# Kernel tuning notes

Hardware: AMD Instinct MI355X
Metric: run time of the kernel (lower is better)

Reference implementation:

```python
import jax, jax.numpy as jnp
import numpy as np

DIM = 128
POS_HID = 64
ATT_HID = DIM * 2
B, N = 4, 512


def _linear_init(key, fan_in, fan_out):
    # mimic torch Linear default init scale: U(-1/sqrt(fan_in), 1/sqrt(fan_in))
    kw, kb = jax.random.split(key)
    bound = 1.0 / np.sqrt(fan_in)
    W = jax.random.uniform(kw, (fan_in, fan_out), minval=-bound, maxval=bound, dtype=jnp.float32)
    b = jax.random.uniform(kb, (fan_out,), minval=-bound, maxval=bound, dtype=jnp.float32)
    return W, b


def setup_inputs() -> dict:
    key = jax.random.key(0)
    ks = jax.random.split(key, 6)
    x = jax.random.normal(ks[0], (B, DIM, N), dtype=jnp.float32)
    pos = jax.random.normal(ks[1], (B, N, 3), dtype=jnp.float32)
    Wqkv, bqkv = _linear_init(ks[2], DIM, DIM * 3)
    pW1, pb1 = _linear_init(ks[3], 3, POS_HID)
    pW2, pb2 = _linear_init(ks[4], POS_HID, DIM)
    k5a, k5b = jax.random.split(ks[5])
    aW1, ab1 = _linear_init(k5a, DIM, ATT_HID)
    aW2, ab2 = _linear_init(k5b, ATT_HID, DIM)
    return {"x": x, "pos": pos, "Wqkv": Wqkv, "bqkv": bqkv,
            "pW1": pW1, "pb1": pb1, "pW2": pW2, "pb2": pb2,
            "aW1": aW1, "ab1": ab1, "aW2": aW2, "ab2": ab2}


def reference(x, pos, Wqkv, bqkv, pW1, pb1, pW2, pb2, aW1, ab1, aW2, ab2):
    # x: [b, d, n] -> [b, n, d]
    xt = jnp.transpose(x, (0, 2, 1))
    qkv = xt @ Wqkv + bqkv                      # [b, n, 3d]
    q, k, v = jnp.split(qkv, 3, axis=-1)        # each [b, n, d]

    # pairwise relative positions: [b, i, j, 3]
    rel_pos = pos[:, :, None, :] - pos[:, None, :, :]
    # pos_mlp: Linear(3, hid) -> ReLU -> Linear(hid, d)
    rel_pos_emb = jax.nn.relu(rel_pos @ pW1 + pb1) @ pW2 + pb2   # [b, i, j, d]

    qk_rel = q[:, :, None, :] - k[:, None, :, :]                 # [b, i, j, d]
    v_ij = v[:, None, :, :] + rel_pos_emb                        # [b, i, j, d]

    # attn_mlp: Linear(d, 2d) -> ReLU -> Linear(2d, d)
    sim = jax.nn.relu((qk_rel + rel_pos_emb) @ aW1 + ab1) @ aW2 + ab2  # [b, i, j, d]
    attn = jax.nn.softmax(sim, axis=2)                           # softmax over j (dim=-2)
    agg = jnp.sum(attn * v_ij, axis=2)                           # [b, i, d]
    return jnp.transpose(agg, (0, 2, 1))                         # [b, d, n]
```

## Files before the change

### kernel.cpp

```cpp
#include <hip/hip_runtime.h>
#include <hip/hip_bf16.h>

#define B_ 4
#define N_ 512
#define D_ 128
#define LOG2E 1.4426950408889634f

typedef __attribute__((ext_vector_type(8))) short bf16x8;
typedef __attribute__((ext_vector_type(4))) short s16x4;
typedef __attribute__((ext_vector_type(4))) float f32x4;

__device__ __forceinline__ f32x4 mfma16(bf16x8 a, bf16x8 b, f32x4 c) {
    return __builtin_amdgcn_mfma_f32_16x16x32_bf16(a, b, c, 0, 0, 0);
}
__device__ __forceinline__ short bf16b(float x) {
    __hip_bfloat16 h = __float2bfloat16(x);
    return *reinterpret_cast<short*>(&h);
}
__device__ __forceinline__ float b2f(short s) {
    unsigned u = ((unsigned)(unsigned short)s) << 16;
    union { unsigned u; float f; } c; c.u = u; return c.f;
}

__global__ void prep_weights_kernel(const float* __restrict__ aW1, const float* __restrict__ aW2,
                                    const float* __restrict__ pW2, const float* __restrict__ pb2,
                                    const float* __restrict__ ab1,
                                    __hip_bfloat16* __restrict__ aW2T, __hip_bfloat16* __restrict__ pW2T,
                                    __hip_bfloat16* __restrict__ W12T, float* __restrict__ cvec) {
    int idx = blockIdx.x * 256 + threadIdx.x;
    if (idx < 128 * 256) {
        int n = idx >> 8, k2 = idx & 255;
        aW2T[idx] = __float2bfloat16(aW2[k2 * 128 + n] * LOG2E);
    }
    if (idx < 128 * 64) {
        int n = idx >> 6, k2 = idx & 63;
        pW2T[idx] = __float2bfloat16(pW2[k2 * 128 + n]);
    }
    if (idx < 256 * 64) {
        int n = idx >> 6, h = idx & 63;
        float s = 0.f;
#pragma unroll 8
        for (int d = 0; d < 128; ++d) s += pW2[h * 128 + d] * aW1[d * 256 + n];
        W12T[idx] = __float2bfloat16(s);
    }
    if (idx < 256) {
        float s = ab1[idx];
#pragma unroll 8
        for (int d = 0; d < 128; ++d) s += pb2[d] * aW1[d * 256 + idx];
        cvec[idx] = s;
    }
}

__global__ void qkv_kernel(const float* __restrict__ x, const float* __restrict__ Wqkv,
                           const float* __restrict__ bqkv,
                           float* __restrict__ q, float* __restrict__ k,
                           short* __restrict__ vb_t) {
    int idx = blockIdx.x * 256 + threadIdx.x;
    int m = idx % 384;
    int g = idx / 384;
    int bn0 = g * 4;
    int b = bn0 >> 9, n0 = bn0 & (N_ - 1);
    const float* xp = x + (b * D_) * N_ + n0;
    float bias = bqkv[m];
    float a0 = bias, a1 = bias, a2 = bias, a3 = bias;
#pragma unroll 4
    for (int d = 0; d < D_; ++d) {
        float wv = Wqkv[d * 384 + m];
        const float4 xv = *reinterpret_cast<const float4*>(xp + d * N_);
        a0 = fmaf(xv.x, wv, a0); a1 = fmaf(xv.y, wv, a1);
        a2 = fmaf(xv.z, wv, a2); a3 = fmaf(xv.w, wv, a3);
    }
    int mm = m & 127;
    if (m < 256) {
        float* dst = (m < 128) ? q : k;
        dst[(bn0 + 0) * D_ + mm] = a0;
        dst[(bn0 + 1) * D_ + mm] = a1;
        dst[(bn0 + 2) * D_ + mm] = a2;
        dst[(bn0 + 3) * D_ + mm] = a3;
    } else {
        int jt = n0 >> 6;
        int mt = (n0 >> 4) & 3;
        int lg = (n0 >> 2) & 3;
        int w  = mm >> 4, lc = mm & 15;
        int l  = lg * 16 + lc;
        s16x4 pk;
        pk[0] = bf16b(a0); pk[1] = bf16b(a1); pk[2] = bf16b(a2); pk[3] = bf16b(a3);
        size_t base = ((((size_t)b * 8 + jt) * 8 + w) * 4 + mt) * 256 + l * 4;
        *(s16x4*)(vb_t + base) = pk;
    }
}

__global__ void qka_kernel(const float* __restrict__ q, const float* __restrict__ k,
                           const float* __restrict__ aW1,
                           float* __restrict__ qa, short* __restrict__ kab_t) {
    int col = threadIdx.x;
    int bn0 = blockIdx.x * 4;
    int b = bn0 >> 9, n0 = bn0 & (N_ - 1);
    const float* qp = q + bn0 * D_;
    const float* kp = k + bn0 * D_;
    float aq0 = 0, aq1 = 0, aq2 = 0, aq3 = 0;
    float ak0 = 0, ak1 = 0, ak2 = 0, ak3 = 0;
#pragma unroll 4
    for (int d = 0; d < D_; ++d) {
        float wv = aW1[d * 256 + col];
        aq0 = fmaf(qp[d], wv, aq0);        ak0 = fmaf(kp[d], wv, ak0);
        aq1 = fmaf(qp[D_ + d], wv, aq1);   ak1 = fmaf(kp[D_ + d], wv, ak1);
        aq2 = fmaf(qp[2*D_ + d], wv, aq2); ak2 = fmaf(kp[2*D_ + d], wv, ak2);
        aq3 = fmaf(qp[3*D_ + d], wv, aq3); ak3 = fmaf(kp[3*D_ + d], wv, ak3);
    }
    qa[(bn0 + 0) * 256 + col] = aq0;
    qa[(bn0 + 1) * 256 + col] = aq1;
    qa[(bn0 + 2) * 256 + col] = aq2;
    qa[(bn0 + 3) * 256 + col] = aq3;
    int jt = n0 >> 6;
    int mt = (n0 >> 4) & 3;
    int lg = (n0 >> 2) & 3;
    int w  = col >> 5, nt = (col >> 4) & 1, lc = col & 15;
    int l  = lg * 16 + lc;
    s16x4 pk;
    pk[0] = bf16b(ak0); pk[1] = bf16b(ak1); pk[2] = bf16b(ak2); pk[3] = bf16b(ak3);
    size_t base = (((((size_t)b * 8 + jt) * 8 + w) * 2 + nt) * 4 + mt) * 256 + l * 4;
    *(s16x4*)(kab_t + base) = pk;
}

__global__ __launch_bounds__(512, 4) void fused_attn_kernel(
    const float* __restrict__ qa, const short* __restrict__ kab_t,
    const short* __restrict__ vb_t,
    const float* __restrict__ pos, const float* __restrict__ pW1, const float* __restrict__ pb1,
    const __hip_bfloat16* __restrict__ pW2T, const float* __restrict__ pb2,
    const __hip_bfloat16* __restrict__ W12T, const float* __restrict__ cvec,
    const __hip_bfloat16* __restrict__ aW2T, const float* __restrict__ ab2,
    float* __restrict__ out)
{
    __shared__ __hip_bfloat16 ph_s[64][72];
    __shared__ __hip_bfloat16 hid_s[64][264];
    __shared__ float pW1_s[192];
    __shared__ float pb1_s[64];

    const int tid = threadIdx.x;
    const int w  = tid >> 6;
    const int l  = tid & 63;
    const int lg = l >> 4;
    const int lc = l & 15;

    const int bi = (blockIdx.x & 7) * 256 + (blockIdx.x >> 3);
    const int b  = bi >> 9;
    const int i  = bi & (N_ - 1);

    if (tid < 192) pW1_s[tid] = pW1[tid];
    else if (tid < 256) pb1_s[tid - 192] = pb1[tid - 192];

    const int col0 = 32 * w + lc;
    const int dcol = 16 * w + lc;

    const float qrow0 = qa[(b * N_ + i) * 256 + col0] + cvec[col0];
    const float qrow1 = qa[(b * N_ + i) * 256 + col0 + 16] + cvec[col0 + 16];
    const float ab2_r = ab2[dcol] * LOG2E;
    const float pb2_r = pb2[dcol];

    const float pi0 = pos[(b * N_ + i) * 3 + 0];
    const float pi1 = pos[(b * N_ + i) * 3 + 1];
    const float pi2 = pos[(b * N_ + i) * 3 + 2];

    bf16x8 bw12[2][2], bw2[8], bwp[2];
    {
        const bf16x8* p12 = (const bf16x8*)W12T;
#pragma unroll
        for (int nt = 0; nt < 2; ++nt)
#pragma unroll
            for (int ks = 0; ks < 2; ++ks)
                bw12[nt][ks] = p12[(32 * w + 16 * nt + lc) * 8 + ks * 4 + lg];
        const bf16x8* p2 = (const bf16x8*)aW2T;
#pragma unroll
        for (int ks = 0; ks < 8; ++ks)
            bw2[ks] = p2[(16 * w + lc) * 32 + ks * 4 + lg];
        const bf16x8* pp = (const bf16x8*)pW2T;
#pragma unroll
        for (int ks = 0; ks < 2; ++ks)
            bwp[ks] = pp[(16 * w + lc) * 8 + ks * 4 + lg];
    }

    float m_run = -1e30f, l_run = 0.f, o_run = 0.f;

    const short* ktp0 = kab_t + (((size_t)b * 8) * 8 + w) * 2048 + l * 4;
    const short* vtp0 = vb_t  + (((size_t)b * 8) * 8 + w) * 1024 + l * 4;

    for (int jt = 0; jt < 8; ++jt) {
        const int jb = jt * 64;
        __syncthreads();

        {
            int jl = tid >> 3;
            int hb = (tid & 7) * 8;
            int j = jb + jl;
            float pj0 = pos[(b * N_ + j) * 3 + 0];
            float pj1 = pos[(b * N_ + j) * 3 + 1];
            float pj2 = pos[(b * N_ + j) * 3 + 2];
            float r0 = pi0 - pj0, r1 = pi1 - pj1, r2 = pi2 - pj2;
            bf16x8 tv;
#pragma unroll
            for (int h = 0; h < 8; ++h) {
                int hh = hb + h;
                float a = pb1_s[hh] + r0 * pW1_s[hh] + r1 * pW1_s[64 + hh] + r2 * pW1_s[128 + hh];
                tv[h] = bf16b(fmaxf(a, 0.f));
            }
            *(bf16x8*)(&ph_s[jl][hb]) = tv;
        }
        __syncthreads();

        const short* ktp = ktp0 + (size_t)jt * 16384;
        const short* vtp = vtp0 + (size_t)jt * 8192;
        s16x4 kv4[2][4], vv4[4];
#pragma unroll
        for (int mt = 0; mt < 4; ++mt)
            vv4[mt] = *(const s16x4*)(vtp + mt * 256);
#pragma unroll
        for (int nt = 0; nt < 2; ++nt)
#pragma unroll
            for (int mt = 0; mt < 4; ++mt)
                kv4[nt][mt] = *(const s16x4*)(ktp + nt * 1024 + mt * 256);

        float vv[4][4];
#pragma unroll
        for (int mt = 0; mt < 4; ++mt) {
            f32x4 acc = {0.f, 0.f, 0.f, 0.f};
#pragma unroll
            for (int ks = 0; ks < 2; ++ks) {
                bf16x8 af = *(const bf16x8*)(&ph_s[mt * 16 + lc][ks * 32 + 8 * lg]);
                acc = mfma16(af, bwp[ks], acc);
            }
#pragma unroll
            for (int r = 0; r < 4; ++r)
                vv[mt][r] = b2f(vv4[mt][r]) + acc[r] + pb2_r;
        }

#pragma unroll
        for (int nt = 0; nt < 2; ++nt) {
            const int colw = col0 + 16 * nt;
            f32x4 acc1[4];
#pragma unroll
            for (int mt = 0; mt < 4; ++mt) acc1[mt] = {0.f, 0.f, 0.f, 0.f};
#pragma unroll
            for (int ks = 0; ks < 2; ++ks)
#pragma unroll
                for (int mt = 0; mt < 4; ++mt) {
                    bf16x8 a = *(const bf16x8*)(&ph_s[mt * 16 + lc][ks * 32 + 8 * lg]);
                    acc1[mt] = mfma16(a, bw12[nt][ks], acc1[mt]);
                }
            const float qv = nt ? qrow1 : qrow0;
#pragma unroll
            for (int mt = 0; mt < 4; ++mt)
#pragma unroll
                for (int r = 0; r < 4; ++r) {
                    int row = mt * 16 + 4 * lg + r;
                    hid_s[row][colw] = __float2bfloat16(
                        fmaxf(acc1[mt][r] + qv - b2f(kv4[nt][mt][r]), 0.f));
                }
        }
        __syncthreads();

        f32x4 acc2[4];
#pragma unroll
        for (int mt = 0; mt < 4; ++mt) acc2[mt] = {0.f, 0.f, 0.f, 0.f};
#pragma unroll
        for (int ks = 0; ks < 8; ++ks)
#pragma unroll
            for (int mt = 0; mt < 4; ++mt) {
                bf16x8 a = *(const bf16x8*)(&hid_s[mt * 16 + lc][ks * 32 + 8 * lg]);
                acc2[mt] = mfma16(a, bw2[ks], acc2[mt]);
            }

        {
            float tmax = -1e30f;
#pragma unroll
            for (int mt = 0; mt < 4; ++mt)
#pragma unroll
                for (int r = 0; r < 4; ++r) {
                    acc2[mt][r] += ab2_r;
                    tmax = fmaxf(tmax, acc2[mt][r]);
                }
            tmax = fmaxf(tmax, __shfl_xor(tmax, 16));
            tmax = fmaxf(tmax, __shfl_xor(tmax, 32));
            float m_new = fmaxf(m_run, tmax);
            float scale = __builtin_amdgcn_exp2f(m_run - m_new);
            l_run *= scale;
            o_run *= scale;
#pragma unroll
            for (int mt = 0; mt < 4; ++mt)
#pragma unroll
                for (int r = 0; r < 4; ++r) {
                    float e = __builtin_amdgcn_exp2f(acc2[mt][r] - m_new);
                    l_run += e;
                    o_run = fmaf(e, vv[mt][r], o_run);
                }
            m_run = m_new;
        }
    }

    float lt = l_run + __shfl_xor(l_run, 16);
    lt += __shfl_xor(lt, 32);
    float ot = o_run + __shfl_xor(o_run, 16);
    ot += __shfl_xor(ot, 32);
    if (lg == 0) out[(b * D_ + dcol) * N_ + i] = ot / lt;
}

extern "C" void kernel_launch(void* const* d_in, const int* in_sizes, int n_in,
                              void* d_out, int out_size, void* d_ws, size_t ws_size,
                              hipStream_t stream) {
    const float* x    = (const float*)d_in[0];
    const float* pos  = (const float*)d_in[1];
    const float* Wqkv = (const float*)d_in[2];
    const float* bqkv = (const float*)d_in[3];
    const float* pW1  = (const float*)d_in[4];
    const float* pb1  = (const float*)d_in[5];
    const float* pW2  = (const float*)d_in[6];
    const float* pb2  = (const float*)d_in[7];
    const float* aW1  = (const float*)d_in[8];
    const float* ab1  = (const float*)d_in[9];
    const float* aW2  = (const float*)d_in[10];
    const float* ab2  = (const float*)d_in[11];
    float* out = (float*)d_out;

    float* q  = (float*)d_ws;
    float* k  = q  + B_ * N_ * D_;
    float* qa = k  + B_ * N_ * D_;
    float* cvec = qa + B_ * N_ * 256;
    short* kab_t = (short*)(cvec + 256);
    short* vb_t  = kab_t + B_ * N_ * 256;
    __hip_bfloat16* aW2T = (__hip_bfloat16*)(vb_t + B_ * N_ * D_);
    __hip_bfloat16* pW2T = aW2T + 128 * 256;
    __hip_bfloat16* W12T = pW2T + 128 * 64;

    hipLaunchKernelGGL(prep_weights_kernel, dim3(128), dim3(256), 0, stream,
                       aW1, aW2, pW2, pb2, ab1, aW2T, pW2T, W12T, cvec);
    hipLaunchKernelGGL(qkv_kernel, dim3(768), dim3(256), 0, stream,
                       x, Wqkv, bqkv, q, k, vb_t);
    hipLaunchKernelGGL(qka_kernel, dim3(512), dim3(256), 0, stream,
                       q, k, aW1, qa, kab_t);
    hipLaunchKernelGGL(fused_attn_kernel, dim3(2048), dim3(512), 0, stream,
                       qa, kab_t, vb_t, pos, pW1, pb1, pW2T, pb2, W12T, cvec, aW2T, ab2, out);
}
```

Measured before the change: 239.7 us.

## Use 32x32 MFMA for second attention GEMM and precompute position projections

Replaces the 16x16x32 MFMAs for the aW2 GEMM and the pos-MLP second layer with 32x32x16 MFMAs, split so each wave handles a 32-row by 32-column tile. Because of that split, each wave keeps a partial online softmax that is merged across rows at the end through shared memory. The v tensor layout is changed to match the 32x32 output fragment, and hidden-tile writes are XOR-swizzled to reduce LDS bank conflicts. A new small kernel precomputes pos·pW1 per point, so the per-pair first layer of the pos MLP becomes a subtraction. The cost is half the aW2 weights being reloaded from global memory every tile and an extra reduction step.

```diff
diff --git a/kernel.cpp b/kernel.cpp
--- a/kernel.cpp
+++ b/kernel.cpp
@@ -9,9 +9,13 @@
 typedef __attribute__((ext_vector_type(8))) short bf16x8;
 typedef __attribute__((ext_vector_type(4))) short s16x4;
 typedef __attribute__((ext_vector_type(4))) float f32x4;
+typedef __attribute__((ext_vector_type(16))) float f32x16;
 
 __device__ __forceinline__ f32x4 mfma16(bf16x8 a, bf16x8 b, f32x4 c) {
     return __builtin_amdgcn_mfma_f32_16x16x32_bf16(a, b, c, 0, 0, 0);
+}
+__device__ __forceinline__ f32x16 mfma32(bf16x8 a, bf16x8 b, f32x16 c) {
+    return __builtin_amdgcn_mfma_f32_32x32x16_bf16(a, b, c, 0, 0, 0);
 }
 __device__ __forceinline__ short bf16b(float x) {
     __hip_bfloat16 h = __float2bfloat16(x);
@@ -49,6 +53,14 @@
         for (int d = 0; d < 128; ++d) s += pb2[d] * aW1[d * 256 + idx];
         cvec[idx] = s;
     }
+}
+
+__global__ void posw_kernel(const float* __restrict__ pos, const float* __restrict__ pW1,
+                            float* __restrict__ posw) {
+    int idx = blockIdx.x * 256 + threadIdx.x;
+    int t = idx >> 6, h = idx & 63;
+    float p0 = pos[t * 3 + 0], p1 = pos[t * 3 + 1], p2 = pos[t * 3 + 2];
+    posw[idx] = p0 * pW1[h] + p1 * pW1[64 + h] + p2 * pW1[128 + h];
 }
 
 __global__ void qkv_kernel(const float* __restrict__ x, const float* __restrict__ Wqkv,
@@ -70,22 +82,26 @@
         a0 = fmaf(xv.x, wv, a0); a1 = fmaf(xv.y, wv, a1);
         a2 = fmaf(xv.z, wv, a2); a3 = fmaf(xv.w, wv, a3);
     }
-    int mm = m & 127;
     if (m < 256) {
+        int mm = m & 127;
         float* dst = (m < 128) ? q : k;
         dst[(bn0 + 0) * D_ + mm] = a0;
         dst[(bn0 + 1) * D_ + mm] = a1;
         dst[(bn0 + 2) * D_ + mm] = a2;
         dst[(bn0 + 3) * D_ + mm] = a3;
     } else {
+        int d = m & 127;
         int jt = n0 >> 6;
-        int mt = (n0 >> 4) & 3;
-        int lg = (n0 >> 2) & 3;
-        int w  = mm >> 4, lc = mm & 15;
-        int l  = lg * 16 + lc;
+        int jr = n0 & 63;
+        int rt = jr >> 5;
+        int jrr = jr & 31;
+        int rb = 4 * (jrr >> 3);
+        int hi = (jrr >> 2) & 1;
+        int lane = (d & 31) + 32 * hi;
+        int ct = d >> 5;
         s16x4 pk;
         pk[0] = bf16b(a0); pk[1] = bf16b(a1); pk[2] = bf16b(a2); pk[3] = bf16b(a3);
-        size_t base = ((((size_t)b * 8 + jt) * 8 + w) * 4 + mt) * 256 + l * 4;
+        size_t base = (size_t)b * 65536 + (size_t)jt * 8192 + ((rt * 4 + ct) * 64 + lane) * 16 + rb;
         *(s16x4*)(vb_t + base) = pk;
     }
 }
@@ -126,7 +142,7 @@
 __global__ __launch_bounds__(512, 4) void fused_attn_kernel(
     const float* __restrict__ qa, const short* __restrict__ kab_t,
     const short* __restrict__ vb_t,
-    const float* __restrict__ pos, const float* __restrict__ pW1, const float* __restrict__ pb1,
+    const float* __restrict__ posw, const float* __restrict__ pb1,
     const __hip_bfloat16* __restrict__ pW2T, const float* __restrict__ pb2,
     const __hip_bfloat16* __restrict__ W12T, const float* __restrict__ cvec,
     const __hip_bfloat16* __restrict__ aW2T, const float* __restrict__ ab2,
@@ -134,174 +150,197 @@
 {
     __shared__ __hip_bfloat16 ph_s[64][72];
     __shared__ __hip_bfloat16 hid_s[64][264];
-    __shared__ float pW1_s[192];
-    __shared__ float pb1_s[64];
+    __shared__ float pwi_s[64];
+    __shared__ float mrg_s[4][32][4];
 
     const int tid = threadIdx.x;
-    const int w  = tid >> 6;
-    const int l  = tid & 63;
-    const int lg = l >> 4;
-    const int lc = l & 15;
+    const int w   = tid >> 6;
+    const int l   = tid & 63;
+    const int lg  = l >> 4;
+    const int lc  = l & 15;
+    const int l31 = l & 31;
+    const int hi  = l >> 5;
+    const int rt  = w >> 2;
+    const int ct  = w & 3;
+    const int gx8 = ((l31 >> 2) & 3) << 3;
 
     const int bi = (blockIdx.x & 7) * 256 + (blockIdx.x >> 3);
     const int b  = bi >> 9;
     const int i  = bi & (N_ - 1);
 
-    if (tid < 192) pW1_s[tid] = pW1[tid];
-    else if (tid < 256) pb1_s[tid - 192] = pb1[tid - 192];
-
-    const int col0 = 32 * w + lc;
-    const int dcol = 16 * w + lc;
+    if (tid < 64) pwi_s[tid] = posw[(size_t)(b * N_ + i) * 64 + tid] + pb1[tid];
+
+    const int col0  = 32 * w + lc;
+    const int dcol2 = 32 * ct + l31;
 
     const float qrow0 = qa[(b * N_ + i) * 256 + col0] + cvec[col0];
     const float qrow1 = qa[(b * N_ + i) * 256 + col0 + 16] + cvec[col0 + 16];
-    const float ab2_r = ab2[dcol] * LOG2E;
-    const float pb2_r = pb2[dcol];
-
-    const float pi0 = pos[(b * N_ + i) * 3 + 0];
-    const float pi1 = pos[(b * N_ + i) * 3 + 1];
-    const float pi2 = pos[(b * N_ + i) * 3 + 2];
-
-    bf16x8 bw12[2][2], bw2[8], bwp[2];
-    {
-        const bf16x8* p12 = (const bf16x8*)W12T;
-#pragma unroll
-        for (int nt = 0; nt < 2; ++nt)
-#pragma unroll
-            for (int ks = 0; ks < 2; ++ks)
-                bw12[nt][ks] = p12[(32 * w + 16 * nt + lc) * 8 + ks * 4 + lg];
-        const bf16x8* p2 = (const bf16x8*)aW2T;
-#pragma unroll
-        for (int ks = 0; ks < 8; ++ks)
-            bw2[ks] = p2[(16 * w + lc) * 32 + ks * 4 + lg];
-        const bf16x8* pp = (const bf16x8*)pW2T;
-#pragma unroll
-        for (int ks = 0; ks < 2; ++ks)
-            bwp[ks] = pp[(16 * w + lc) * 8 + ks * 4 + lg];
-    }
+    const float ab2_r = ab2[dcol2] * LOG2E;
+    const float pb2_r = pb2[dcol2];
+
+    const __hip_bfloat16* a2base = aW2T + (size_t)dcol2 * 256 + 8 * hi;
+    bf16x8 bw2lo[8];
+#pragma unroll
+    for (int ks = 0; ks < 8; ++ks)
+        bw2lo[ks] = *(const bf16x8*)(a2base + 16 * ks);
+    bf16x8 bw12[2][2];
+#pragma unroll
+    for (int nt = 0; nt < 2; ++nt)
+#pragma unroll
+        for (int k2 = 0; k2 < 2; ++k2)
+            bw12[nt][k2] = *(const bf16x8*)(W12T + (size_t)(32 * w + 16 * nt + lc) * 64 + k2 * 32 + 8 * lg);
 
     float m_run = -1e30f, l_run = 0.f, o_run = 0.f;
 
-    const short* ktp0 = kab_t + (((size_t)b * 8) * 8 + w) * 2048 + l * 4;
-    const short* vtp0 = vb_t  + (((size_t)b * 8) * 8 + w) * 1024 + l * 4;
+    const short* ktp0 = kab_t + (size_t)b * 131072 + w * 2048 + l * 4;
+    const short* vtp0 = vb_t + (size_t)b * 65536 + ((rt * 4 + ct) * 64 + l) * 16;
+
+    __syncthreads();
 
     for (int jt = 0; jt < 8; ++jt) {
         const int jb = jt * 64;
+
+        {
+            const int jl = tid >> 3;
+            const int hb = (tid & 7) * 8;
+            const float* pj = posw + (size_t)(b * N_ + jb + jl) * 64 + hb;
+            float4 x0 = *(const float4*)pj;
+            float4 x1 = *(const float4*)(pj + 4);
+            bf16x8 tv;
+            tv[0] = bf16b(fmaxf(pwi_s[hb + 0] - x0.x, 0.f));
+            tv[1] = bf16b(fmaxf(pwi_s[hb + 1] - x0.y, 0.f));
+            tv[2] = bf16b(fmaxf(pwi_s[hb + 2] - x0.z, 0.f));
+            tv[3] = bf16b(fmaxf(pwi_s[hb + 3] - x0.w, 0.f));
+            tv[4] = bf16b(fmaxf(pwi_s[hb + 4] - x1.x, 0.f));
+            tv[5] = bf16b(fmaxf(pwi_s[hb + 5] - x1.y, 0.f));
+            tv[6] = bf16b(fmaxf(pwi_s[hb + 6] - x1.z, 0.f));
+            tv[7] = bf16b(fmaxf(pwi_s[hb + 7] - x1.w, 0.f));
+            *(bf16x8*)(&ph_s[jl][hb]) = tv;
+        }
         __syncthreads();
 
-        {
-            int jl = tid >> 3;
-            int hb = (tid & 7) * 8;
-            int j = jb + jl;
-            float pj0 = pos[(b * N_ + j) * 3 + 0];
-            float pj1 = pos[(b * N_ + j) * 3 + 1];
-            float pj2 = pos[(b * N_ + j) * 3 + 2];
-            float r0 = pi0 - pj0, r1 = pi1 - pj1, r2 = pi2 - pj2;
-            bf16x8 tv;
-#pragma unroll
-            for (int h = 0; h < 8; ++h) {
-                int hh = hb + h;
-                float a = pb1_s[hh] + r0 * pW1_s[hh] + r1 * pW1_s[64 + hh] + r2 * pW1_s[128 + hh];
-                tv[h] = bf16b(fmaxf(a, 0.f));
-            }
-            *(bf16x8*)(&ph_s[jl][hb]) = tv;
+        float vv[16];
+        {
+            const short* vtp = vtp0 + (size_t)jt * 8192;
+            s16x4 vb4[4];
+#pragma unroll
+            for (int q4 = 0; q4 < 4; ++q4)
+                vb4[q4] = *(const s16x4*)(vtp + 4 * q4);
+            bf16x8 bwp[4];
+            const __hip_bfloat16* ppb = pW2T + (size_t)dcol2 * 64 + 8 * hi;
+#pragma unroll
+            for (int ks = 0; ks < 4; ++ks)
+                bwp[ks] = *(const bf16x8*)(ppb + 16 * ks);
+            f32x16 accr = {0.f,0.f,0.f,0.f,0.f,0.f,0.f,0.f,0.f,0.f,0.f,0.f,0.f,0.f,0.f,0.f};
+#pragma unroll
+            for (int ks = 0; ks < 4; ++ks) {
+                bf16x8 a = *(const bf16x8*)(&ph_s[32 * rt + l31][16 * ks + 8 * hi]);
+                accr = mfma32(a, bwp[ks], accr);
+            }
+#pragma unroll
+            for (int r = 0; r < 16; ++r)
+                vv[r] = accr[r] + b2f(vb4[r >> 2][r & 3]) + pb2_r;
+        }
+
+        {
+            const short* ktp = ktp0 + (size_t)jt * 16384;
+            s16x4 kv[2][4];
+#pragma unroll
+            for (int nt = 0; nt < 2; ++nt)
+#pragma unroll
+                for (int mt = 0; mt < 4; ++mt)
+                    kv[nt][mt] = *(const s16x4*)(ktp + nt * 1024 + mt * 256);
+#pragma unroll
+            for (int mt = 0; mt < 4; ++mt) {
+                bf16x8 a0 = *(const bf16x8*)(&ph_s[mt * 16 + lc][8 * lg]);
+                bf16x8 a1 = *(const bf16x8*)(&ph_s[mt * 16 + lc][32 + 8 * lg]);
+#pragma unroll
+                for (int nt = 0; nt < 2; ++nt) {
+                    f32x4 acc = {0.f, 0.f, 0.f, 0.f};
+                    acc = mfma16(a0, bw12[nt][0], acc);
+                    acc = mfma16(a1, bw12[nt][1], acc);
+                    const float qv = nt ? qrow1 : qrow0;
+                    const int colw = 32 * w + (((16 * nt + lc) ^ (8 * lg)) & 31);
+#pragma unroll
+                    for (int r = 0; r < 4; ++r) {
+                        int row = mt * 16 + 4 * lg + r;
+                        hid_s[row][colw] = __float2bfloat16(
+                            fmaxf(acc[r] + qv - b2f(kv[nt][mt][r]), 0.f));
+                    }
+                }
+            }
         }
         __syncthreads();
 
-        const short* ktp = ktp0 + (size_t)jt * 16384;
-        const short* vtp = vtp0 + (size_t)jt * 8192;
-        s16x4 kv4[2][4], vv4[4];
-#pragma unroll
-        for (int mt = 0; mt < 4; ++mt)
-            vv4[mt] = *(const s16x4*)(vtp + mt * 256);
-#pragma unroll
-        for (int nt = 0; nt < 2; ++nt)
-#pragma unroll
-            for (int mt = 0; mt < 4; ++mt)
-                kv4[nt][mt] = *(const s16x4*)(ktp + nt * 1024 + mt * 256);
-
-        float vv[4][4];
-#pragma unroll
-        for (int mt = 0; mt < 4; ++mt) {
-            f32x4 acc = {0.f, 0.f, 0.f, 0.f};
-#pragma unroll
-            for (int ks = 0; ks < 2; ++ks) {
-                bf16x8 af = *(const bf16x8*)(&ph_s[mt * 16 + lc][ks * 32 + 8 * lg]);
-                acc = mfma16(af, bwp[ks], acc);
-            }
-#pragma unroll
-            for (int r = 0; r < 4; ++r)
-                vv[mt][r] = b2f(vv4[mt][r]) + acc[r] + pb2_r;
-        }
-
-#pragma unroll
-        for (int nt = 0; nt < 2; ++nt) {
-            const int colw = col0 + 16 * nt;
-            f32x4 acc1[4];
-#pragma unroll
-            for (int mt = 0; mt < 4; ++mt) acc1[mt] = {0.f, 0.f, 0.f, 0.f};
-#pragma unroll
-            for (int ks = 0; ks < 2; ++ks)
-#pragma unroll
-                for (int mt = 0; mt < 4; ++mt) {
-                    bf16x8 a = *(const bf16x8*)(&ph_s[mt * 16 + lc][ks * 32 + 8 * lg]);
-                    acc1[mt] = mfma16(a, bw12[nt][ks], acc1[mt]);
-                }
-            const float qv = nt ? qrow1 : qrow0;
-#pragma unroll
-            for (int mt = 0; mt < 4; ++mt)
-#pragma unroll
-                for (int r = 0; r < 4; ++r) {
-                    int row = mt * 16 + 4 * lg + r;
-                    hid_s[row][colw] = __float2bfloat16(
-                        fmaxf(acc1[mt][r] + qv - b2f(kv4[nt][mt][r]), 0.f));
-                }
-        }
-        __syncthreads();
-
-        f32x4 acc2[4];
-#pragma unroll
-        for (int mt = 0; mt < 4; ++mt) acc2[mt] = {0.f, 0.f, 0.f, 0.f};
-#pragma unroll
-        for (int ks = 0; ks < 8; ++ks)
-#pragma unroll
-            for (int mt = 0; mt < 4; ++mt) {
-                bf16x8 a = *(const bf16x8*)(&hid_s[mt * 16 + lc][ks * 32 + 8 * lg]);
-                acc2[mt] = mfma16(a, bw2[ks], acc2[mt]);
-            }
-
-        {
-            float tmax = -1e30f;
-#pragma unroll
-            for (int mt = 0; mt < 4; ++mt)
-#pragma unroll
-                for (int r = 0; r < 4; ++r) {
-                    acc2[mt][r] += ab2_r;
-                    tmax = fmaxf(tmax, acc2[mt][r]);
-                }
-            tmax = fmaxf(tmax, __shfl_xor(tmax, 16));
-            tmax = fmaxf(tmax, __shfl_xor(tmax, 32));
+        f32x16 acc2 = {0.f,0.f,0.f,0.f,0.f,0.f,0.f,0.f,0.f,0.f,0.f,0.f,0.f,0.f,0.f,0.f};
+        {
+            const short* hrow = (const short*)&hid_s[32 * rt + l31][0];
+            bf16x8 bh[8];
+#pragma unroll
+            for (int ks = 0; ks < 8; ++ks)
+                bh[ks] = *(const bf16x8*)(a2base + 16 * (ks + 8));
+#pragma unroll
+            for (int ks = 0; ks < 8; ++ks) {
+                bf16x8 a = *(const bf16x8*)(hrow + ((16 * ks + 8 * hi) ^ gx8));
+                acc2 = mfma32(a, bw2lo[ks], acc2);
+            }
+#pragma unroll
+            for (int ks = 0; ks < 8; ++ks) {
+                bf16x8 a = *(const bf16x8*)(hrow + ((16 * (ks + 8) + 8 * hi) ^ gx8));
+                acc2 = mfma32(a, bh[ks], acc2);
+            }
+        }
+
+        {
+            float s[16];
+#pragma unroll
+            for (int r = 0; r < 16; ++r) s[r] = acc2[r] + ab2_r;
+            float t8[8];
+#pragma unroll
+            for (int r = 0; r < 8; ++r) t8[r] = fmaxf(s[r], s[r + 8]);
+            float t4a = fmaxf(t8[0], t8[4]), t4b = fmaxf(t8[1], t8[5]);
+            float t4c = fmaxf(t8[2], t8[6]), t4d = fmaxf(t8[3], t8[7]);
+            float tmax = fmaxf(fmaxf(t4a, t4b), fmaxf(t4c, t4d));
             float m_new = fmaxf(m_run, tmax);
             float scale = __builtin_amdgcn_exp2f(m_run - m_new);
             l_run *= scale;
             o_run *= scale;
 #pragma unroll
-            for (int mt = 0; mt < 4; ++mt)
-#pragma unroll
-                for (int r = 0; r < 4; ++r) {
-                    float e = __builtin_amdgcn_exp2f(acc2[mt][r] - m_new);
-                    l_run += e;
-                    o_run = fmaf(e, vv[mt][r], o_run);
-                }
+            for (int r = 0; r < 16; ++r) {
+                float e = __builtin_amdgcn_exp2f(s[r] - m_new);
+                l_run += e;
+                o_run = fmaf(e, vv[r], o_run);
+            }
             m_run = m_new;
         }
     }
 
-    float lt = l_run + __shfl_xor(l_run, 16);
-    lt += __shfl_xor(lt, 32);
-    float ot = o_run + __shfl_xor(o_run, 16);
-    ot += __shfl_xor(ot, 32);
-    if (lg == 0) out[(b * D_ + dcol) * N_ + i] = ot / lt;
+    float m2 = __shfl_xor(m_run, 32);
+    float l2 = __shfl_xor(l_run, 32);
+    float o2 = __shfl_xor(o_run, 32);
+    float M1 = fmaxf(m_run, m2);
+    float e1 = __builtin_amdgcn_exp2f(m_run - M1);
+    float e2 = __builtin_amdgcn_exp2f(m2 - M1);
+    float L1 = l_run * e1 + l2 * e2;
+    float O1 = o_run * e1 + o2 * e2;
+
+    if (rt == 1 && hi == 0) {
+        mrg_s[ct][l31][0] = M1;
+        mrg_s[ct][l31][1] = L1;
+        mrg_s[ct][l31][2] = O1;
+    }
+    __syncthreads();
+    if (rt == 0 && hi == 0) {
+        float Mb = mrg_s[ct][l31][0];
+        float Lb = mrg_s[ct][l31][1];
+        float Ob = mrg_s[ct][l31][2];
+        float M = fmaxf(M1, Mb);
+        float ea = __builtin_amdgcn_exp2f(M1 - M);
+        float eb = __builtin_amdgcn_exp2f(Mb - M);
+        float L = L1 * ea + Lb * eb;
+        float O = O1 * ea + Ob * eb;
+        out[((size_t)b * D_ + dcol2) * N_ + i] = O / L;
+    }
 }
 
 extern "C" void kernel_launch(void* const* d_in, const int* in_sizes, int n_in,
@@ -321,10 +360,11 @@
     const float* ab2  = (const float*)d_in[11];
     float* out = (float*)d_out;
 
-    float* q  = (float*)d_ws;
-    float* k  = q  + B_ * N_ * D_;
-    float* qa = k  + B_ * N_ * D_;
-    float* cvec = qa + B_ * N_ * 256;
+    float* q    = (float*)d_ws;
+    float* k    = q  + B_ * N_ * D_;
+    float* qa   = k  + B_ * N_ * D_;
+    float* posw = qa + B_ * N_ * 256;
+    float* cvec = posw + B_ * N_ * 64;
     short* kab_t = (short*)(cvec + 256);
     short* vb_t  = kab_t + B_ * N_ * 256;
     __hip_bfloat16* aW2T = (__hip_bfloat16*)(vb_t + B_ * N_ * D_);
@@ -333,10 +373,12 @@
 
     hipLaunchKernelGGL(prep_weights_kernel, dim3(128), dim3(256), 0, stream,
                        aW1, aW2, pW2, pb2, ab1, aW2T, pW2T, W12T, cvec);
+    hipLaunchKernelGGL(posw_kernel, dim3(512), dim3(256), 0, stream,
+                       pos, pW1, posw);
     hipLaunchKernelGGL(qkv_kernel, dim3(768), dim3(256), 0, stream,
                        x, Wqkv, bqkv, q, k, vb_t);
     hipLaunchKernelGGL(qka_kernel, dim3(512), dim3(256), 0, stream,
                        q, k, aW1, qa, kab_t);
     hipLaunchKernelGGL(fused_attn_kernel, dim3(2048), dim3(512), 0, stream,
-                       qa, kab_t, vb_t, pos, pW1, pb1, pW2T, pb2, W12T, cvec, aW2T, ab2, out);
-}
+                       qa, kab_t, vb_t, posw, pb1, pW2T, pb2, W12T, cvec, aW2T, ab2, out);
+}
```

Result: slower. 377.1 us (+57.3%).
